# Kernel optimization log

Hardware: AMD Instinct MI355X
Metric: run time of the kernel (lower is better)

Reference implementation:

```python
import jax, jax.numpy as jnp
import numpy as np

B, L, D = 8, 4096, 1024


def setup_inputs() -> dict:
    key = jax.random.key(0)
    k1, k2, k3 = jax.random.split(key, 3)
    states = jax.random.normal(k1, (B, L, D), dtype=jnp.float32)
    reasoning_mask = jax.random.randint(k2, (B, L), 0, 2).astype(jnp.float32)
    result_token_positions = jax.random.randint(k3, (B,), 0, L, dtype=jnp.int64)
    return {
        "states": states,
        "reasoning_mask": reasoning_mask,
        "result_token_positions": result_token_positions,
    }


def reference(states, reasoning_mask, result_token_positions):
    # states: [B, L, D]; reasoning_mask: [B, L]; result_token_positions: [B]
    Bs, Ls, Ds = states.shape
    # ||s_t - s_{t-1}||  -> [B, L-1]
    deltas = jnp.linalg.norm(states[:, 1:, :] - states[:, :-1, :], axis=-1)
    # relu of consecutive delta increase -> [B, L-2]
    delta_increase = jax.nn.relu(deltas[:, 1:] - deltas[:, :-1])
    mask = reasoning_mask[:, 2:]  # [B, L-2]
    # approach weight: dist = max(rp - t - 2, 0); weight = 2 + (5-dist)*0.5 if dist < 5 else 1
    t = jnp.arange(Ls - 2)
    dist = jnp.maximum(result_token_positions[:, None] - t[None, :] - 2, 0)  # [B, L-2]
    approach_weight = jnp.where(
        dist < 5,
        jnp.float32(2.0) + (5 - dist).astype(states.dtype) * jnp.float32(0.5),
        jnp.float32(1.0),
    )
    weighted = delta_increase * mask * approach_weight
    return weighted.sum() / (mask.sum() + 1e-9)
```

## Files before the change

### kernel.cpp

```cpp
#include <hip/hip_runtime.h>
#include <math.h>

#define BB 8
#define LL 4096
#define DD 1024
#define LM1 4095
#define LM2 4094
#define CHUNK 32
#define NCHUNK 128

__global__ __launch_bounds__(256) void delta_kernel(const float* __restrict__ states,
                                                    float* __restrict__ delta) {
    const int bid = blockIdx.x;
    const int b = bid / NCHUNK;
    const int c = bid % NCHUNK;
    const int i0 = c * CHUNK;
    const int iend = (i0 + CHUNK < LM1) ? (i0 + CHUNK) : LM1;
    const int tid = threadIdx.x;
    const int lane = tid & 63;
    const int wid = tid >> 6;

    const float4* base = (const float4*)states + (size_t)b * LL * (DD / 4) + tid;

    __shared__ float lds[4];

    float4 prev = base[(size_t)i0 * (DD / 4)];
    for (int i = i0; i < iend; ++i) {
        float4 cur = base[(size_t)(i + 1) * (DD / 4)];
        float dx = cur.x - prev.x;
        float dy = cur.y - prev.y;
        float dz = cur.z - prev.z;
        float dw = cur.w - prev.w;
        float s = dx * dx + dy * dy + dz * dz + dw * dw;
        #pragma unroll
        for (int off = 32; off > 0; off >>= 1) s += __shfl_down(s, off);
        if (lane == 0) lds[wid] = s;
        __syncthreads();
        if (tid == 0) delta[b * LM1 + i] = sqrtf(lds[0] + lds[1] + lds[2] + lds[3]);
        __syncthreads();
        prev = cur;
    }
}

__global__ __launch_bounds__(256) void weighted_kernel(const float* __restrict__ delta,
                                                       const float* __restrict__ rmask,
                                                       const int* __restrict__ rpos,
                                                       float* __restrict__ pnum,
                                                       float* __restrict__ pden) {
    const int tid = threadIdx.x;
    const int gid = blockIdx.x * blockDim.x + tid;
    const int stride = gridDim.x * blockDim.x;
    const int lane = tid & 63;
    const int wid = tid >> 6;

    float num = 0.0f, den = 0.0f;
    for (int b = 0; b < BB; ++b) {
        const int rp = rpos[b];
        const float* __restrict__ db = delta + b * LM1;
        const float* __restrict__ mb = rmask + b * LL + 2;
        for (int t = gid; t < LM2; t += stride) {
            float inc = db[t + 1] - db[t];
            inc = inc > 0.0f ? inc : 0.0f;
            float m = mb[t];
            int dist = rp - t - 2;
            if (dist < 0) dist = 0;
            float w = (dist < 5) ? (2.0f + (float)(5 - dist) * 0.5f) : 1.0f;
            num += inc * m * w;
            den += m;
        }
    }
    #pragma unroll
    for (int off = 32; off > 0; off >>= 1) {
        num += __shfl_down(num, off);
        den += __shfl_down(den, off);
    }
    __shared__ float ln[4], ld[4];
    if (lane == 0) { ln[wid] = num; ld[wid] = den; }
    __syncthreads();
    if (tid == 0) {
        pnum[blockIdx.x] = ln[0] + ln[1] + ln[2] + ln[3];
        pden[blockIdx.x] = ld[0] + ld[1] + ld[2] + ld[3];
    }
}

__global__ __launch_bounds__(64) void final_kernel(const float* __restrict__ pnum,
                                                   const float* __restrict__ pden,
                                                   float* __restrict__ out) {
    const int lane = threadIdx.x;
    float n = pnum[lane];
    float d = pden[lane];
    #pragma unroll
    for (int off = 32; off > 0; off >>= 1) {
        n += __shfl_down(n, off);
        d += __shfl_down(d, off);
    }
    if (lane == 0) out[0] = n / (d + 1e-9f);
}

extern "C" void kernel_launch(void* const* d_in, const int* in_sizes, int n_in,
                              void* d_out, int out_size, void* d_ws, size_t ws_size,
                              hipStream_t stream) {
    const float* states = (const float*)d_in[0];
    const float* rmask  = (const float*)d_in[1];
    const int*   rpos   = (const int*)d_in[2];
    float* out = (float*)d_out;

    float* ws    = (float*)d_ws;
    float* delta = ws;
    float* pnum  = ws + 32768;
    float* pden  = ws + 32768 + 64;

    delta_kernel<<<BB * NCHUNK, 256, 0, stream>>>(states, delta);
    weighted_kernel<<<64, 256, 0, stream>>>(delta, rmask, rpos, pnum, pden);
    final_kernel<<<1, 64, 0, stream>>>(pnum, pden, out);
}
```

Measured before the change: 200.4 us.

## Fuse delta and weighted reduction into one wave-per-chunk kernel

Replaces the block-per-chunk delta kernel and the separate weighted-sum kernel with a single kernel. Each 64-lane wave handles a 16-step chunk, loads 18 rows with four float4 per lane, and keeps per-row partial sums in registers. A butterfly reduction then gives each lane one delta, and the delta increase is formed by a lane shuffle. This removes the two __syncthreads per row, the delta round trip through global memory, and one launch. The cost is re-reading two boundary rows per chunk and higher register use.

New measurement: 198.3 us (median of 2 runs). About the same (-1.0%).

```diff
diff --git a/kernel.cpp b/kernel.cpp
--- a/kernel.cpp
+++ b/kernel.cpp
@@ -6,69 +6,85 @@
 #define DD 1024
 #define LM1 4095
 #define LM2 4094
-#define CHUNK 32
-#define NCHUNK 128
+#define CHUNK 16
+#define NDELTA 17
+#define ROWS 18
+#define NCH 256
+#define NBLK 512
 
-__global__ __launch_bounds__(256) void delta_kernel(const float* __restrict__ states,
-                                                    float* __restrict__ delta) {
-    const int bid = blockIdx.x;
-    const int b = bid / NCHUNK;
-    const int c = bid % NCHUNK;
-    const int i0 = c * CHUNK;
-    const int iend = (i0 + CHUNK < LM1) ? (i0 + CHUNK) : LM1;
+__global__ __launch_bounds__(256) void fused_kernel(const float* __restrict__ states,
+                                                    const float* __restrict__ rmask,
+                                                    const int* __restrict__ rpos,
+                                                    float* __restrict__ pnum,
+                                                    float* __restrict__ pden) {
     const int tid = threadIdx.x;
     const int lane = tid & 63;
     const int wid = tid >> 6;
+    const int w = blockIdx.x * 4 + wid;
+    const int b = w >> 8;
+    const int c = w & (NCH - 1);
+    const int t0 = c * CHUNK;
 
-    const float4* base = (const float4*)states + (size_t)b * LL * (DD / 4) + tid;
+    const float4* base = (const float4*)states + (size_t)b * (LL * (DD / 4)) + lane;
 
-    __shared__ float lds[4];
+    float partial[NDELTA];
 
-    float4 prev = base[(size_t)i0 * (DD / 4)];
-    for (int i = i0; i < iend; ++i) {
-        float4 cur = base[(size_t)(i + 1) * (DD / 4)];
-        float dx = cur.x - prev.x;
-        float dy = cur.y - prev.y;
-        float dz = cur.z - prev.z;
-        float dw = cur.w - prev.w;
-        float s = dx * dx + dy * dy + dz * dz + dw * dw;
+    float4 p0, p1, p2, p3;
+    {
+        const float4* rp_ = base + (size_t)t0 * (DD / 4);
+        p0 = rp_[0]; p1 = rp_[64]; p2 = rp_[128]; p3 = rp_[192];
+    }
+    #pragma unroll
+    for (int r = 1; r < ROWS; ++r) {
+        int row = t0 + r;
+        if (row > LL - 1) row = LL - 1;
+        const float4* rp_ = base + (size_t)row * (DD / 4);
+        float4 c0 = rp_[0], c1 = rp_[64], c2 = rp_[128], c3 = rp_[192];
+        float s = 0.0f, d;
+        d = c0.x - p0.x; s += d * d;
+        d = c0.y - p0.y; s += d * d;
+        d = c0.z - p0.z; s += d * d;
+        d = c0.w - p0.w; s += d * d;
+        d = c1.x - p1.x; s += d * d;
+        d = c1.y - p1.y; s += d * d;
+        d = c1.z - p1.z; s += d * d;
+        d = c1.w - p1.w; s += d * d;
+        d = c2.x - p2.x; s += d * d;
+        d = c2.y - p2.y; s += d * d;
+        d = c2.z - p2.z; s += d * d;
+        d = c2.w - p2.w; s += d * d;
+        d = c3.x - p3.x; s += d * d;
+        d = c3.y - p3.y; s += d * d;
+        d = c3.z - p3.z; s += d * d;
+        d = c3.w - p3.w; s += d * d;
+        partial[r - 1] = s;
+        p0 = c0; p1 = c1; p2 = c2; p3 = c3;
+    }
+
+    float dval = 0.0f;
+    #pragma unroll
+    for (int d2 = 0; d2 < NDELTA; ++d2) {
+        float s = partial[d2];
         #pragma unroll
-        for (int off = 32; off > 0; off >>= 1) s += __shfl_down(s, off);
-        if (lane == 0) lds[wid] = s;
-        __syncthreads();
-        if (tid == 0) delta[b * LM1 + i] = sqrtf(lds[0] + lds[1] + lds[2] + lds[3]);
-        __syncthreads();
-        prev = cur;
+        for (int off = 1; off < 64; off <<= 1) s += __shfl_xor(s, off);
+        if (lane == d2) dval = sqrtf(s);
     }
-}
+    float dnext = __shfl_down(dval, 1);
 
-__global__ __launch_bounds__(256) void weighted_kernel(const float* __restrict__ delta,
-                                                       const float* __restrict__ rmask,
-                                                       const int* __restrict__ rpos,
-                                                       float* __restrict__ pnum,
-                                                       float* __restrict__ pden) {
-    const int tid = threadIdx.x;
-    const int gid = blockIdx.x * blockDim.x + tid;
-    const int stride = gridDim.x * blockDim.x;
-    const int lane = tid & 63;
-    const int wid = tid >> 6;
+    const int t = t0 + lane;
+    const bool valid = (lane < CHUNK) && (t < LM2);
+    float inc = dnext - dval;
+    inc = inc > 0.0f ? inc : 0.0f;
+    int midx = b * LL + t + 2;
+    if (midx > BB * LL - 1) midx = BB * LL - 1;
+    float m = valid ? rmask[midx] : 0.0f;
+    const int rp = rpos[b];
+    int dist = rp - t - 2;
+    if (dist < 0) dist = 0;
+    const float wgt = (dist < 5) ? (2.0f + (float)(5 - dist) * 0.5f) : 1.0f;
+    float num = valid ? inc * m * wgt : 0.0f;
+    float den = m;
 
-    float num = 0.0f, den = 0.0f;
-    for (int b = 0; b < BB; ++b) {
-        const int rp = rpos[b];
-        const float* __restrict__ db = delta + b * LM1;
-        const float* __restrict__ mb = rmask + b * LL + 2;
-        for (int t = gid; t < LM2; t += stride) {
-            float inc = db[t + 1] - db[t];
-            inc = inc > 0.0f ? inc : 0.0f;
-            float m = mb[t];
-            int dist = rp - t - 2;
-            if (dist < 0) dist = 0;
-            float w = (dist < 5) ? (2.0f + (float)(5 - dist) * 0.5f) : 1.0f;
-            num += inc * m * w;
-            den += m;
-        }
-    }
     #pragma unroll
     for (int off = 32; off > 0; off >>= 1) {
         num += __shfl_down(num, off);
@@ -83,18 +99,28 @@
     }
 }
 
-__global__ __launch_bounds__(64) void final_kernel(const float* __restrict__ pnum,
-                                                   const float* __restrict__ pden,
-                                                   float* __restrict__ out) {
-    const int lane = threadIdx.x;
-    float n = pnum[lane];
-    float d = pden[lane];
+__global__ __launch_bounds__(512) void final_kernel(const float* __restrict__ pnum,
+                                                    const float* __restrict__ pden,
+                                                    float* __restrict__ out) {
+    const int tid = threadIdx.x;
+    const int lane = tid & 63;
+    const int wid = tid >> 6;
+    float n = pnum[tid];
+    float d = pden[tid];
     #pragma unroll
     for (int off = 32; off > 0; off >>= 1) {
         n += __shfl_down(n, off);
         d += __shfl_down(d, off);
     }
-    if (lane == 0) out[0] = n / (d + 1e-9f);
+    __shared__ float ln[8], ld[8];
+    if (lane == 0) { ln[wid] = n; ld[wid] = d; }
+    __syncthreads();
+    if (tid == 0) {
+        float N = 0.0f, D = 0.0f;
+        #pragma unroll
+        for (int i = 0; i < 8; ++i) { N += ln[i]; D += ld[i]; }
+        out[0] = N / (D + 1e-9f);
+    }
 }
 
 extern "C" void kernel_launch(void* const* d_in, const int* in_sizes, int n_in,
@@ -105,12 +131,10 @@
     const int*   rpos   = (const int*)d_in[2];
     float* out = (float*)d_out;
 
-    float* ws    = (float*)d_ws;
-    float* delta = ws;
-    float* pnum  = ws + 32768;
-    float* pden  = ws + 32768 + 64;
+    float* ws   = (float*)d_ws;
+    float* pnum = ws;
+    float* pden = ws + NBLK;
 
-    delta_kernel<<<BB * NCHUNK, 256, 0, stream>>>(states, delta);
-    weighted_kernel<<<64, 256, 0, stream>>>(delta, rmask, rpos, pnum, pden);
-    final_kernel<<<1, 64, 0, stream>>>(pnum, pden, out);
+    fused_kernel<<<NBLK, 256, 0, stream>>>(states, rmask, rpos, pnum, pden);
+    final_kernel<<<1, 512, 0, stream>>>(pnum, pden, out);
 }
```
